# Kernel optimization log

Hardware: AMD Instinct MI355X
Metric: run time of the kernel (lower is better)

Reference implementation:

```python
import jax, jax.numpy as jnp
import numpy as np

N_NODES = 50000
N_EDGES = 800000
NODE_DIM = 128
EDGE_DIM = 2
HID = 512
SLOPE = 0.15  # LeakyReLU negative slope


def _leaky(x):
    return jnp.where(x > 0, x, SLOPE * x)


def _lin(key, fan_in, fan_out, bias=True):
    s = 1.0 / np.sqrt(fan_in)
    k1, k2 = jax.random.split(key)
    W = jax.random.uniform(k1, (fan_in, fan_out), jnp.float32, -s, s)
    if not bias:
        return W
    b = jax.random.uniform(k2, (fan_out,), jnp.float32, -s, s)
    return W, b


def setup_inputs() -> dict:
    key = jax.random.key(0)
    ks = jax.random.split(key, 12)
    x = jax.random.normal(ks[0], (N_NODES, NODE_DIM), jnp.float32)
    edge_index = jax.random.randint(ks[1], (2, N_EDGES), 0, N_NODES, jnp.int32)
    edge_attr = jax.random.normal(ks[2], (N_EDGES, EDGE_DIM), jnp.float32)
    We, be = _lin(ks[3], EDGE_DIM, HID)
    # SAGEConv: out = lin_l(mean_agg(x_j)) + lin_r(x_i); lin_l has bias, lin_r does not
    W1l, b1 = _lin(ks[4], NODE_DIM, HID)
    W1r = _lin(ks[5], NODE_DIM, HID, bias=False)
    W2l, b2 = _lin(ks[6], HID, 256)
    W2r = _lin(ks[7], HID, 256, bias=False)
    W3l, b3 = _lin(ks[8], 256, 64)
    W3r = _lin(ks[9], 256, 64, bias=False)
    Wp, bp = _lin(ks[10], 64, 32)
    kf1, kf2 = jax.random.split(ks[11])
    Wf1, bf1 = _lin(kf1, 32, 32)
    Wf2, bf2 = _lin(kf2, 32, 2)
    return dict(x=x, edge_index=edge_index, edge_attr=edge_attr,
                We=We, be=be, W1l=W1l, b1=b1, W1r=W1r,
                W2l=W2l, b2=b2, W2r=W2r, W3l=W3l, b3=b3, W3r=W3r,
                Wp=Wp, bp=bp, Wf1=Wf1, bf1=bf1, Wf2=Wf2, bf2=bf2)


def _sage(h, src, dst, Wl, bl, Wr):
    # mean aggregation of source-node features at destination nodes
    n = h.shape[0]
    summed = jax.ops.segment_sum(h[src], dst, num_segments=n)          # [N, d]
    cnt = jax.ops.segment_sum(jnp.ones((src.shape[0],), h.dtype), dst, num_segments=n)
    mean = summed / jnp.maximum(cnt, 1.0)[:, None]
    return mean @ Wl + bl + h @ Wr


def reference(x, edge_index, edge_attr, We, be, W1l, b1, W1r,
              W2l, b2, W2r, W3l, b3, W3r, Wp, bp, Wf1, bf1, Wf2, bf2):
    src, dst = edge_index[0], edge_index[1]
    _edge_feats = edge_attr @ We + be  # computed in the original forward but never used downstream
    h = _leaky(_sage(x, src, dst, W1l, b1, W1r))   # dropout is identity in eval
    h = _leaky(_sage(h, src, dst, W2l, b2, W2r))
    h = _leaky(_sage(h, src, dst, W3l, b3, W3r))
    h = h @ Wp + bp                                 # pre_fc
    h = _leaky(h @ Wf1 + bf1)                       # classifier (Linear fallback)
    return h @ Wf2 + bf2                            # [N, 2]
```

## Files before the change

kernel.cpp:

```cpp
#include <hip/hip_runtime.h>
#include <hip/hip_fp16.h>

#define N_NODES 50000
#define N_EDGES 800000
#define SLOPE 0.15f

typedef unsigned short u16;
typedef __attribute__((ext_vector_type(8))) _Float16 f16x8;
typedef __attribute__((ext_vector_type(2))) _Float16 h16x2;
typedef __attribute__((ext_vector_type(4))) float f32x4;

static __device__ __forceinline__ float leaky(float v) { return v > 0.f ? v : SLOPE * v; }

static __device__ __forceinline__ u16 f2h(float v) {
    return __builtin_bit_cast(u16, __float2half(v));
}

static __device__ __forceinline__ float dot2acc(unsigned int u, float c) {
    h16x2 one = {(_Float16)1.0f, (_Float16)1.0f};
    return __builtin_amdgcn_fdot2(__builtin_bit_cast(h16x2, u), one, c, false);
}

static __device__ __forceinline__ void async_load16(const u16* g, u16* l) {
    __builtin_amdgcn_global_load_lds(
        (const __attribute__((address_space(1))) unsigned int*)g,
        (__attribute__((address_space(3))) unsigned int*)l, 16, 0, 0);
}

__global__ void k_prep(const int* __restrict__ dst, int* __restrict__ cnt,
                       int* __restrict__ erank,
                       const float* __restrict__ x, u16* __restrict__ xp,
                       const float* __restrict__ W1l, const float* __restrict__ W1r,
                       const float* __restrict__ W2l, const float* __restrict__ W2r,
                       const float* __restrict__ W3l, const float* __restrict__ W3r,
                       u16* w1lp, u16* w1rp, u16* w2cp, u16* w3cp) {
    int b = blockIdx.x, tid = threadIdx.x;
    if (b < 3125) {
        int e = b * 256 + tid;
        if (e < N_EDGES) erank[e] = atomicAdd(&cnt[dst[e]], 1);
        return;
    }
    b -= 3125;
    if (b < 6250) {
        int i = b * 256 + tid;
        if (i >= N_NODES * 32) return;
        float4 v = ((const float4*)x)[i];
        ((ushort4*)xp)[i] = make_ushort4(f2h(v.x), f2h(v.y), f2h(v.z), f2h(v.w));
        return;
    }
    b -= 6250;
    const float* W; u16* op; int K, N;
    if (b < 256)       { W = W1l; op = w1lp; K = 128; N = 512; }
    else if (b < 512)  { W = W1r; op = w1rp; K = 128; N = 512; b -= 256; }
    else if (b < 1024) { W = W2l; op = w2cp; K = 512; N = 256; b -= 512; }
    else if (b < 1536) { W = W2r; op = w2cp + 256 * 512; K = 512; N = 256; b -= 1024; }
    else if (b < 1600) { W = W3l; op = w3cp; K = 256; N = 64; b -= 1536; }
    else               { W = W3r; op = w3cp + 64 * 256; K = 256; N = 64; b -= 1600; }
    int i = b * 256 + tid;
    if (i >= K * N) return;
    int k = i / N, n = i - k * N;
    op[(size_t)n * K + k] = f2h(W[i]);
}

__global__ __launch_bounds__(1024) void k_scan1(const int* __restrict__ cnt,
                                                int* __restrict__ offs,
                                                int* __restrict__ bsum) {
    __shared__ int wsum[16];
    int tid = threadIdx.x, lane = tid & 63, wv = tid >> 6;
    int i = blockIdx.x * 1024 + tid;
    int c = (i < N_NODES) ? cnt[i] : 0;
    int orig = (c + 15) & ~15;
    int v = orig;
#pragma unroll
    for (int d = 1; d < 64; d <<= 1) {
        int t = __shfl_up(v, d, 64);
        if (lane >= d) v += t;
    }
    if (lane == 63) wsum[wv] = v;
    __syncthreads();
    if (wv == 0) {
        int s = (lane < 16) ? wsum[lane] : 0;
#pragma unroll
        for (int d = 1; d < 16; d <<= 1) {
            int t = __shfl_up(s, d, 64);
            if (lane >= d) s += t;
        }
        if (lane < 16) wsum[lane] = s;
        if (lane == 15) bsum[blockIdx.x] = s;
    }
    __syncthreads();
    int wpre = (wv == 0) ? 0 : wsum[wv - 1];
    if (i < N_NODES) offs[i] = v + wpre - orig;
}

__global__ void k_scan3(const int* __restrict__ cnt, int* __restrict__ offs,
                        float* __restrict__ inv, int* __restrict__ pssrc,
                        const int* __restrict__ bsum, int nb) {
    __shared__ int sb[64];
    int tid = threadIdx.x;
    if (tid < 64) {
        int v = (tid < nb) ? bsum[tid] : 0;
        int s = v;
#pragma unroll
        for (int d = 1; d < 64; d <<= 1) {
            int t = __shfl_up(s, d, 64);
            if (tid >= d) s += t;
        }
        sb[tid] = s - v;
        if (blockIdx.x == 0 && tid == nb - 1) offs[N_NODES] = s;
    }
    __syncthreads();
    int i = blockIdx.x * 256 + tid;
    if (i >= N_NODES) return;
    int c = cnt[i];
    int o = offs[i] + sb[i >> 10];
    offs[i] = o;
    inv[i] = 1.0f / (float)(c > 1 ? c : 1);
    int cp = (c + 15) & ~15;
    for (int j = c; j < cp; ++j) pssrc[o + j] = N_NODES;
}

__global__ void k_fill(const int* __restrict__ src, const int* __restrict__ dst,
                       const int* __restrict__ erank, const int* __restrict__ poffs,
                       int* __restrict__ pssrc) {
    int t = blockIdx.x * 256 + threadIdx.x;
    int e = t * 4;
    if (e + 3 >= N_EDGES) {
        for (; e < N_EDGES; ++e) pssrc[poffs[dst[e]] + erank[e]] = src[e];
        return;
    }
    int4 d4 = *(const int4*)&dst[e];
    int4 s4 = *(const int4*)&src[e];
    int4 r4 = *(const int4*)&erank[e];
    int p0 = poffs[d4.x] + r4.x;
    int p1 = poffs[d4.y] + r4.y;
    int p2 = poffs[d4.z] + r4.z;
    int p3 = poffs[d4.w] + r4.w;
    pssrc[p0] = s4.x;
    pssrc[p1] = s4.y;
    pssrc[p2] = s4.z;
    pssrc[p3] = s4.w;
}

template <int STRIDE, int EPI, int LPE, int U>
__global__ __launch_bounds__(256) void k_agg(const u16* __restrict__ tbl,
                                             const int* __restrict__ poffs,
                                             const int* __restrict__ pssrc,
                                             const float* __restrict__ inv,
                                             const u16* __restrict__ y,
                                             const float* __restrict__ bias,
                                             u16* __restrict__ outh,
                                             float* __restrict__ outf) {
    constexpr int G = 64 / LPE;
    int wid = (blockIdx.x * 256 + threadIdx.x) >> 6;
    if (wid >= N_NODES) return;
    int lane = threadIdx.x & 63;
    int g = lane / LPE;
    int cl = lane % LPE;
    int beg = poffs[wid], end = poffs[wid + 1];
    const u16* colbase = tbl + cl * 8;
    float acc[8] = {};
    for (int e = beg + g * U; e < end; e += G * U) {
        int idx[U];
        if constexpr (U == 4) {
            int4 t4 = *(const int4*)&pssrc[e];
            idx[0] = t4.x; idx[1] = t4.y; idx[2] = t4.z; idx[3] = t4.w;
        } else {
            int2 t2 = *(const int2*)&pssrc[e];
            idx[0] = t2.x; idx[1] = t2.y;
        }
        uint4 rv[U];
#pragma unroll
        for (int j = 0; j < U; ++j)
            rv[j] = *(const uint4*)(colbase + (size_t)idx[j] * STRIDE);
#pragma unroll
        for (int p = 0; p < U / 2; ++p) {
            const unsigned int* a = (const unsigned int*)&rv[2 * p];
            const unsigned int* b = (const unsigned int*)&rv[2 * p + 1];
#pragma unroll
            for (int t = 0; t < 4; ++t) {
                unsigned int lo = __builtin_amdgcn_perm(b[t], a[t], 0x05040100u);
                unsigned int hi = __builtin_amdgcn_perm(b[t], a[t], 0x07060302u);
                acc[2 * t + 0] = dot2acc(lo, acc[2 * t + 0]);
                acc[2 * t + 1] = dot2acc(hi, acc[2 * t + 1]);
            }
        }
    }
#pragma unroll
    for (int m = LPE; m < 64; m <<= 1)
#pragma unroll
        for (int t = 0; t < 8; ++t) acc[t] += __shfl_xor(acc[t], m, 64);
    if (g != 0) return;
    float wv = inv[wid];
    const size_t ob = (size_t)wid * STRIDE + cl * 8;
    float v[8];
    if constexpr (EPI == 0) {
#pragma unroll
        for (int t = 0; t < 8; ++t) v[t] = acc[t] * wv;
    } else {
        uint4 yv4 = *(const uint4*)(y + ob);
        const __half2* yp = (const __half2*)&yv4;
        float4 b0 = *(const float4*)(bias + cl * 8);
        float4 b1 = *(const float4*)(bias + cl * 8 + 4);
        float bb[8] = {b0.x, b0.y, b0.z, b0.w, b1.x, b1.y, b1.z, b1.w};
#pragma unroll
        for (int t = 0; t < 4; ++t) {
            float2 f = __half22float2(yp[t]);
            v[t * 2 + 0] = leaky(acc[t * 2 + 0] * wv + f.x + bb[t * 2 + 0]);
            v[t * 2 + 1] = leaky(acc[t * 2 + 1] * wv + f.y + bb[t * 2 + 1]);
        }
    }
    if constexpr (EPI == 3) {
        *(float4*)(outf + ob)     = make_float4(v[0], v[1], v[2], v[3]);
        *(float4*)(outf + ob + 4) = make_float4(v[4], v[5], v[6], v[7]);
    } else {
        *(ushort4*)(outh + ob)     = make_ushort4(f2h(v[0]), f2h(v[1]), f2h(v[2]), f2h(v[3]));
        *(ushort4*)(outh + ob + 4) = make_ushort4(f2h(v[4]), f2h(v[5]), f2h(v[6]), f2h(v[7]));
    }
}

__global__ __launch_bounds__(256, 4) void k_gemm_f(
    int M, int nct,
    const u16* __restrict__ A1, const u16* __restrict__ B1, int K1,
    const u16* __restrict__ A2, const u16* __restrict__ B2, int K2,
    const float* __restrict__ bias, int act, int colsplit,
    u16* __restrict__ out1h, int n1, u16* __restrict__ out2h, int n2) {
    __shared__ u16 Ash[2][4096], Bsh[2][4096];
    const int tid = threadIdx.x;
    const int lane = tid & 63;
    const int w = tid >> 6;
    const int wm = w & 1, wn = w >> 1;
    const int fr = lane & 15;
    const int q = lane >> 4;

    const int mT = (M + 127) >> 7;
    const int lin = blockIdx.x;
    const int grp = lin / (8 * nct);
    const int idx = lin - grp * (8 * nct);
    const int ct = idx >> 3;
    const int s8 = idx & 7;
    const int rowt = grp * 8 + s8;
    if (rowt >= mT) return;
    const int brow = rowt * 128;
    const int bcol = ct * 128;

    const int T1 = K1 >> 5, T = T1 + (K2 >> 5);

    const int c0 = (w * 2 + 0) * 64 + lane;
    const int c1 = (w * 2 + 1) * 64 + lane;
    const int r0 = c0 >> 2, g0 = (c0 & 3) ^ ((r0 >> 1) & 3);
    const int r1 = c1 >> 2, g1 = (c1 & 3) ^ ((r1 >> 1) & 3);
    int ar0 = brow + r0; if (ar0 >= M) ar0 = M - 1;
    int ar1 = brow + r1; if (ar1 >= M) ar1 = M - 1;
    const int br0 = bcol + r0, br1 = bcol + r1;
    const int ub0 = (w * 2 + 0) * 512;
    const int ub1 = (w * 2 + 1) * 512;

    auto stage = [&](int kt, int buf) {
        const u16 *A, *B; int K, k0;
        if (kt < T1) { A = A1; B = B1; K = K1; k0 = kt * 32; }
        else         { A = A2; B = B2; K = K2; k0 = (kt - T1) * 32; }
        async_load16(A + (size_t)ar0 * K + k0 + g0 * 8, &Ash[buf][ub0]);
        async_load16(A + (size_t)ar1 * K + k0 + g1 * 8, &Ash[buf][ub1]);
        async_load16(B + (size_t)br0 * K + k0 + g0 * 8, &Bsh[buf][ub0]);
        async_load16(B + (size_t)br1 * K + k0 + g1 * 8, &Bsh[buf][ub1]);
    };

    f32x4 acc[4][4] = {};

    stage(0, 0);
    __syncthreads();

    int cur = 0;
    for (int kt = 0; kt < T; ++kt) {
        if (kt + 1 < T) stage(kt + 1, cur ^ 1);
        f16x8 fa[4], fb[4];
#pragma unroll
        for (int rt = 0; rt < 4; ++rt) {
            int row = wm * 64 + rt * 16 + fr;
            int ad = row * 32 + ((q ^ ((row >> 1) & 3)) * 8);
            fa[rt] = __builtin_bit_cast(f16x8, *(const uint4*)&Ash[cur][ad]);
        }
#pragma unroll
        for (int ctf = 0; ctf < 4; ++ctf) {
            int row = wn * 64 + ctf * 16 + fr;
            int ad = row * 32 + ((q ^ ((row >> 1) & 3)) * 8);
            fb[ctf] = __builtin_bit_cast(f16x8, *(const uint4*)&Bsh[cur][ad]);
        }
#pragma unroll
        for (int rt = 0; rt < 4; ++rt)
#pragma unroll
            for (int ctf = 0; ctf < 4; ++ctf)
                acc[rt][ctf] = __builtin_amdgcn_mfma_f32_16x16x32_f16(fa[rt], fb[ctf], acc[rt][ctf], 0, 0, 0);
        if (kt + 1 < T) __syncthreads();
        cur ^= 1;
    }

#pragma unroll
    for (int rt = 0; rt < 4; ++rt) {
        int rowb = brow + wm * 64 + rt * 16 + q * 4;
#pragma unroll
        for (int ctf = 0; ctf < 4; ++ctf) {
            int col = bcol + wn * 64 + ctf * 16 + fr;
            float b = bias ? bias[col] : 0.f;
#pragma unroll
            for (int r = 0; r < 4; ++r) {
                int row = rowb + r;
                if (row >= M) continue;
                float v = acc[rt][ctf][r] + b;
                if (act) v = leaky(v);
                if (col < colsplit) out1h[(size_t)row * n1 + col] = f2h(v);
                else                out2h[(size_t)row * n2 + (col - colsplit)] = f2h(v);
            }
        }
    }
}

__global__ __launch_bounds__(256) void k_head(const float* __restrict__ h3,
                                              const float* __restrict__ Wp, const float* __restrict__ bp,
                                              const float* __restrict__ Wf1, const float* __restrict__ bf1,
                                              const float* __restrict__ Wf2, const float* __restrict__ bf2,
                                              float* __restrict__ out) {
    __shared__ float sWp[64 * 32], sW1[32 * 32], sW2[32 * 2];
    __shared__ float sbp[32], sb1[32], sb2[2];
    int tid = threadIdx.x;
    for (int i = tid; i < 64 * 32; i += 256) sWp[i] = Wp[i];
    for (int i = tid; i < 32 * 32; i += 256) sW1[i] = Wf1[i];
    for (int i = tid; i < 64; i += 256) sW2[i] = Wf2[i];
    if (tid < 32) { sbp[tid] = bp[tid]; sb1[tid] = bf1[tid]; }
    if (tid < 2) sb2[tid] = bf2[tid];
    __syncthreads();
    int row = blockIdx.x * 256 + tid;
    if (row >= N_NODES) return;
    const float4* h4v = (const float4*)(h3 + (size_t)row * 64);
    float xr[64];
#pragma unroll
    for (int i = 0; i < 16; ++i) {
        float4 v = h4v[i];
        xr[i * 4 + 0] = v.x; xr[i * 4 + 1] = v.y;
        xr[i * 4 + 2] = v.z; xr[i * 4 + 3] = v.w;
    }
    float h4[32];
    for (int o = 0; o < 32; ++o) {
        float s = sbp[o];
#pragma unroll
        for (int i = 0; i < 64; ++i) s += xr[i] * sWp[i * 32 + o];
        h4[o] = s;
    }
    float h5[32];
    for (int o = 0; o < 32; ++o) {
        float s = sb1[o];
#pragma unroll
        for (int i = 0; i < 32; ++i) s += h4[i] * sW1[i * 32 + o];
        h5[o] = leaky(s);
    }
#pragma unroll
    for (int o = 0; o < 2; ++o) {
        float s = sb2[o];
#pragma unroll
        for (int i = 0; i < 32; ++i) s += h5[i] * sW2[i * 2 + o];
        out[(size_t)row * 2 + o] = s;
    }
}

extern "C" void kernel_launch(void* const* d_in, const int* in_sizes, int n_in,
                              void* d_out, int out_size, void* d_ws, size_t ws_size,
                              hipStream_t stream) {
    const float* x   = (const float*)d_in[0];
    const int*   ei  = (const int*)d_in[1];
    const float* W1l = (const float*)d_in[5];
    const float* b1  = (const float*)d_in[6];
    const float* W1r = (const float*)d_in[7];
    const float* W2l = (const float*)d_in[8];
    const float* b2  = (const float*)d_in[9];
    const float* W2r = (const float*)d_in[10];
    const float* W3l = (const float*)d_in[11];
    const float* b3  = (const float*)d_in[12];
    const float* W3r = (const float*)d_in[13];
    const float* Wp  = (const float*)d_in[14];
    const float* bp  = (const float*)d_in[15];
    const float* Wf1 = (const float*)d_in[16];
    const float* bf1 = (const float*)d_in[17];
    const float* Wf2 = (const float*)d_in[18];
    const float* bf2 = (const float*)d_in[19];
    float* out = (float*)d_out;
    (void)in_sizes; (void)n_in; (void)out_size; (void)ws_size;

    const int* src = ei;
    const int* dst = ei + N_EDGES;

    char* base = (char*)d_ws;
    size_t off = 0;
    auto alloc = [&](size_t bytes) -> void* {
        void* r = base + off;
        off = (off + bytes + 255) & ~(size_t)255;
        return r;
    };
    const size_t NN = N_NODES;
    int*   cnt    = (int*)alloc(NN * 4);
    int*   offs   = (int*)alloc((NN + 1) * 4);
    float* inv    = (float*)alloc(NN * 4);
    int*   bsum   = (int*)alloc(64 * 4);
    int*   erank  = (int*)alloc((size_t)N_EDGES * 4);
    int*   pssrc  = (int*)alloc((size_t)(N_EDGES + 16 * N_NODES) * 4);
    u16* w1lp = (u16*)alloc(128 * 512 * 2);
    u16* w1rp = (u16*)alloc(128 * 512 * 2);
    u16* w2cp = (u16*)alloc(512 * 512 * 2);
    u16* w3cp = (u16*)alloc(128 * 256 * 2);
    u16* xp  = (u16*)alloc((NN + 1) * 128 * 2);
    u16* axp = (u16*)alloc(NN * 128 * 2);
    u16* h1p = (u16*)alloc(NN * 512 * 2);
    u16* z2h = (u16*)alloc((NN + 1) * 256 * 2);
    u16* y2h = (u16*)alloc(NN * 256 * 2);
    u16* h2p = (u16*)alloc(NN * 256 * 2);
    u16* z3h = (u16*)alloc((NN + 1) * 64 * 2);
    u16* y3h = (u16*)alloc(NN * 64 * 2);
    float* h3f = (float*)alloc(NN * 64 * 4);

    hipMemsetAsync(cnt, 0, NN * 4, stream);
    hipMemsetAsync(xp + NN * 128, 0, 128 * 2, stream);
    hipMemsetAsync(z2h + NN * 256, 0, 256 * 2, stream);
    hipMemsetAsync(z3h + NN * 64, 0, 64 * 2, stream);
    k_prep<<<3125 + 6250 + 1664, 256, 0, stream>>>(dst, cnt, erank, x, xp,
        W1l, W1r, W2l, W2r, W3l, W3r, w1lp, w1rp, w2cp, w3cp);
    const int nb = (N_NODES + 1023) / 1024;
    k_scan1<<<nb, 1024, 0, stream>>>(cnt, offs, bsum);
    k_scan3<<<(N_NODES + 255) / 256, 256, 0, stream>>>(cnt, offs, inv, pssrc, bsum, nb);
    k_fill<<<(N_EDGES / 4 + 255) / 256, 256, 0, stream>>>(src, dst, erank, offs, pssrc);

    const int aggGrid = (N_NODES + 3) / 4;
    const int mT = (N_NODES + 127) / 128;
    const int grid4 = ((mT + 7) / 8) * 32;
    const int grid1 = ((mT + 7) / 8) * 8;

    k_agg<128, 0, 16, 4><<<aggGrid, 256, 0, stream>>>(
        xp, offs, pssrc, inv, nullptr, nullptr, axp, nullptr);
    k_gemm_f<<<grid4, 256, 0, stream>>>(N_NODES, 4,
        axp, w1lp, 128, xp, w1rp, 128, b1, 1, 512, h1p, 512, nullptr, 0);

    k_gemm_f<<<grid4, 256, 0, stream>>>(N_NODES, 4,
        h1p, w2cp, 512, nullptr, nullptr, 0, nullptr, 0, 256, z2h, 256, y2h, 256);
    k_agg<256, 2, 32, 4><<<aggGrid, 256, 0, stream>>>(
        z2h, offs, pssrc, inv, y2h, b2, h2p, nullptr);

    k_gemm_f<<<grid1, 256, 0, stream>>>(N_NODES, 1,
        h2p, w3cp, 256, nullptr, nullptr, 0, nullptr, 0, 64, z3h, 64, y3h, 64);
    k_agg<64, 3, 8, 2><<<aggGrid, 256, 0, stream>>>(
        z3h, offs, pssrc, inv, y3h, b3, nullptr, h3f);

    k_head<<<(N_NODES + 255) / 256, 256, 0, stream>>>(h3f,
        Wp, bp, Wf1, bf1, Wf2, bf2, out);
}
```

Before: 427.5 us.

## Load GEMM MFMA fragments directly from global memory, skipping LDS staging

```diff
diff --git a/kernel.cpp b/kernel.cpp
--- a/kernel.cpp
+++ b/kernel.cpp
@@ -19,12 +19,6 @@
 static __device__ __forceinline__ float dot2acc(unsigned int u, float c) {
     h16x2 one = {(_Float16)1.0f, (_Float16)1.0f};
     return __builtin_amdgcn_fdot2(__builtin_bit_cast(h16x2, u), one, c, false);
-}
-
-static __device__ __forceinline__ void async_load16(const u16* g, u16* l) {
-    __builtin_amdgcn_global_load_lds(
-        (const __attribute__((address_space(1))) unsigned int*)g,
-        (__attribute__((address_space(3))) unsigned int*)l, 16, 0, 0);
 }
 
 __global__ void k_prep(const int* __restrict__ dst, int* __restrict__ cnt,
@@ -219,13 +213,42 @@
     }
 }
 
-__global__ __launch_bounds__(256, 4) void k_gemm_f(
+template <int K>
+static __device__ __forceinline__ void gemm_seg(
+    const u16* __restrict__ A, const u16* __restrict__ B, int M,
+    int brow, int bcol, int wm, int wn, int fr, int q, f32x4 (&acc)[4][4]) {
+    const u16* pA[4]; const u16* pB[4];
+#pragma unroll
+    for (int t = 0; t < 4; ++t) {
+        int ar = brow + wm * 64 + t * 16 + fr; if (ar >= M) ar = M - 1;
+        pA[t] = A + (size_t)ar * K + q * 8;
+        int br = bcol + wn * 64 + t * 16 + fr;
+        pB[t] = B + (size_t)br * K + q * 8;
+    }
+#pragma unroll 4
+    for (int kt = 0; kt < K / 32; ++kt) {
+        f16x8 fa[4], fb[4];
+#pragma unroll
+        for (int t = 0; t < 4; ++t)
+            fa[t] = __builtin_bit_cast(f16x8, *(const uint4*)(pA[t] + kt * 32));
+#pragma unroll
+        for (int t = 0; t < 4; ++t)
+            fb[t] = __builtin_bit_cast(f16x8, *(const uint4*)(pB[t] + kt * 32));
+#pragma unroll
+        for (int rt = 0; rt < 4; ++rt)
+#pragma unroll
+            for (int cf = 0; cf < 4; ++cf)
+                acc[rt][cf] = __builtin_amdgcn_mfma_f32_16x16x32_f16(fa[rt], fb[cf], acc[rt][cf], 0, 0, 0);
+    }
+}
+
+template <int K1, int K2>
+__global__ __launch_bounds__(256, 4) void k_gemm_d(
     int M, int nct,
-    const u16* __restrict__ A1, const u16* __restrict__ B1, int K1,
-    const u16* __restrict__ A2, const u16* __restrict__ B2, int K2,
+    const u16* __restrict__ A1, const u16* __restrict__ B1,
+    const u16* __restrict__ A2, const u16* __restrict__ B2,
     const float* __restrict__ bias, int act, int colsplit,
     u16* __restrict__ out1h, int n1, u16* __restrict__ out2h, int n2) {
-    __shared__ u16 Ash[2][4096], Bsh[2][4096];
     const int tid = threadIdx.x;
     const int lane = tid & 63;
     const int w = tid >> 6;
@@ -244,70 +267,23 @@
     const int brow = rowt * 128;
     const int bcol = ct * 128;
 
-    const int T1 = K1 >> 5, T = T1 + (K2 >> 5);
-
-    const int c0 = (w * 2 + 0) * 64 + lane;
-    const int c1 = (w * 2 + 1) * 64 + lane;
-    const int r0 = c0 >> 2, g0 = (c0 & 3) ^ ((r0 >> 1) & 3);
-    const int r1 = c1 >> 2, g1 = (c1 & 3) ^ ((r1 >> 1) & 3);
-    int ar0 = brow + r0; if (ar0 >= M) ar0 = M - 1;
-    int ar1 = brow + r1; if (ar1 >= M) ar1 = M - 1;
-    const int br0 = bcol + r0, br1 = bcol + r1;
-    const int ub0 = (w * 2 + 0) * 512;
-    const int ub1 = (w * 2 + 1) * 512;
-
-    auto stage = [&](int kt, int buf) {
-        const u16 *A, *B; int K, k0;
-        if (kt < T1) { A = A1; B = B1; K = K1; k0 = kt * 32; }
-        else         { A = A2; B = B2; K = K2; k0 = (kt - T1) * 32; }
-        async_load16(A + (size_t)ar0 * K + k0 + g0 * 8, &Ash[buf][ub0]);
-        async_load16(A + (size_t)ar1 * K + k0 + g1 * 8, &Ash[buf][ub1]);
-        async_load16(B + (size_t)br0 * K + k0 + g0 * 8, &Bsh[buf][ub0]);
-        async_load16(B + (size_t)br1 * K + k0 + g1 * 8, &Bsh[buf][ub1]);
-    };
-
     f32x4 acc[4][4] = {};
-
-    stage(0, 0);
-    __syncthreads();
-
-    int cur = 0;
-    for (int kt = 0; kt < T; ++kt) {
-        if (kt + 1 < T) stage(kt + 1, cur ^ 1);
-        f16x8 fa[4], fb[4];
-#pragma unroll
-        for (int rt = 0; rt < 4; ++rt) {
-            int row = wm * 64 + rt * 16 + fr;
-            int ad = row * 32 + ((q ^ ((row >> 1) & 3)) * 8);
-            fa[rt] = __builtin_bit_cast(f16x8, *(const uint4*)&Ash[cur][ad]);
-        }
-#pragma unroll
-        for (int ctf = 0; ctf < 4; ++ctf) {
-            int row = wn * 64 + ctf * 16 + fr;
-            int ad = row * 32 + ((q ^ ((row >> 1) & 3)) * 8);
-            fb[ctf] = __builtin_bit_cast(f16x8, *(const uint4*)&Bsh[cur][ad]);
-        }
-#pragma unroll
-        for (int rt = 0; rt < 4; ++rt)
-#pragma unroll
-            for (int ctf = 0; ctf < 4; ++ctf)
-                acc[rt][ctf] = __builtin_amdgcn_mfma_f32_16x16x32_f16(fa[rt], fb[ctf], acc[rt][ctf], 0, 0, 0);
-        if (kt + 1 < T) __syncthreads();
-        cur ^= 1;
-    }
+    gemm_seg<K1>(A1, B1, M, brow, bcol, wm, wn, fr, q, acc);
+    if constexpr (K2 > 0)
+        gemm_seg<K2>(A2, B2, M, brow, bcol, wm, wn, fr, q, acc);
 
 #pragma unroll
     for (int rt = 0; rt < 4; ++rt) {
         int rowb = brow + wm * 64 + rt * 16 + q * 4;
 #pragma unroll
-        for (int ctf = 0; ctf < 4; ++ctf) {
-            int col = bcol + wn * 64 + ctf * 16 + fr;
+        for (int cf = 0; cf < 4; ++cf) {
+            int col = bcol + wn * 64 + cf * 16 + fr;
             float b = bias ? bias[col] : 0.f;
 #pragma unroll
             for (int r = 0; r < 4; ++r) {
                 int row = rowb + r;
                 if (row >= M) continue;
-                float v = acc[rt][ctf][r] + b;
+                float v = acc[rt][cf][r] + b;
                 if (act) v = leaky(v);
                 if (col < colsplit) out1h[(size_t)row * n1 + col] = f2h(v);
                 else                out2h[(size_t)row * n2 + (col - colsplit)] = f2h(v);
@@ -430,21 +406,21 @@
 
     const int aggGrid = (N_NODES + 3) / 4;
     const int mT = (N_NODES + 127) / 128;
-    const int grid4 = ((mT + 7) / 8) * 32;
+    const int grid4 = ((mT + 7) / 8) * 8 * 4;
     const int grid1 = ((mT + 7) / 8) * 8;
 
     k_agg<128, 0, 16, 4><<<aggGrid, 256, 0, stream>>>(
         xp, offs, pssrc, inv, nullptr, nullptr, axp, nullptr);
-    k_gemm_f<<<grid4, 256, 0, stream>>>(N_NODES, 4,
-        axp, w1lp, 128, xp, w1rp, 128, b1, 1, 512, h1p, 512, nullptr, 0);
-
-    k_gemm_f<<<grid4, 256, 0, stream>>>(N_NODES, 4,
-        h1p, w2cp, 512, nullptr, nullptr, 0, nullptr, 0, 256, z2h, 256, y2h, 256);
+    k_gemm_d<128, 128><<<grid4, 256, 0, stream>>>(N_NODES, 4,
+        axp, w1lp, xp, w1rp, b1, 1, 512, h1p, 512, nullptr, 0);
+
+    k_gemm_d<512, 0><<<grid4, 256, 0, stream>>>(N_NODES, 4,
+        h1p, w2cp, nullptr, nullptr, nullptr, 0, 256, z2h, 256, y2h, 256);
     k_agg<256, 2, 32, 4><<<aggGrid, 256, 0, stream>>>(
         z2h, offs, pssrc, inv, y2h, b2, h2p, nullptr);
 
-    k_gemm_f<<<grid1, 256, 0, stream>>>(N_NODES, 1,
-        h2p, w3cp, 256, nullptr, nullptr, 0, nullptr, 0, 64, z3h, 64, y3h, 64);
+    k_gemm_d<256, 0><<<grid1, 256, 0, stream>>>(N_NODES, 1,
+        h2p, w3cp, nullptr, nullptr, nullptr, 0, 64, z3h, 64, y3h, 64);
     k_agg<64, 3, 8, 2><<<aggGrid, 256, 0, stream>>>(
         z3h, offs, pssrc, inv, y3h, b3, nullptr, h3f);
 
```

Result: slower. 533.3 us (+24.7%).
